# Optimization experiments

Hardware: AMD Instinct MI355X
Metric: run time of the kernel (lower is better)

The kernel has to match this reference:

```python
import jax, jax.numpy as jnp
import numpy as np

N_CLASSES = 91

def setup_inputs() -> dict:
    key = jax.random.key(0)
    k1, k2 = jax.random.split(key)
    B, H, W = 32, 1024, 1024
    inputs = jax.random.randint(k1, (B, H, W), 0, N_CLASSES, dtype=jnp.int32)
    targets = jax.random.randint(k2, (B, H, W), 0, N_CLASSES, dtype=jnp.int32)
    smooth = jnp.ones((1,), dtype=jnp.float32)  # original default smooth=1
    return {"inputs": inputs, "targets": targets, "smooth": smooth}

def reference(inputs, targets, smooth):
    # Single-pass histogram formulation of the original 91-iteration loop.
    B = inputs.shape[0]
    x = inputs.reshape(B, -1)   # [B, N] int labels
    t = targets.reshape(B, -1)  # [B, N]
    rows = jnp.arange(B)[:, None]
    # per-class counts: cnt_x[b,c] = #pixels with x==c (== a.sum per class)
    cnt_x = jnp.zeros((B, N_CLASSES), jnp.float32).at[rows, x].add(1.0)
    cnt_t = jnp.zeros((B, N_CLASSES), jnp.float32).at[rows, t].add(1.0)
    # intersection[b,c] = #pixels with x==t==c; route mismatches to a dump bin
    match = jnp.where(x == t, x, N_CLASSES)
    inter = jnp.zeros((B, N_CLASSES + 1), jnp.float32).at[rows, match].add(1.0)[:, :N_CLASSES]
    union = cnt_x + cnt_t - inter  # total - intersection
    s = smooth[0]
    iou = (inter + s) / (union + s)  # [B, C]
    return iou.mean(axis=1)          # sum_IoU / n_classes, shape [B]
```

## Files before the change

### kernel.cpp

```cpp
#include <hip/hip_runtime.h>

#define NC 91
#define NBIN 182
#define NCOL 8
#define NB 32
#define HW (1024 * 1024)
#define PIX_PER_BLOCK 4096

__global__ __launch_bounds__(256) void hist_kernel(const int* __restrict__ x,
                                                   const int* __restrict__ t,
                                                   int* __restrict__ g_hist) {
    __shared__ int s_h[4][NBIN * NCOL];

    const int tid = threadIdx.x;
    int* sf = &s_h[0][0];
    for (int i = tid; i < 4 * NBIN * NCOL; i += 256) sf[i] = 0;
    __syncthreads();

    const int wave = tid >> 6;
    const int col  = tid & (NCOL - 1);
    int* h = s_h[wave];

    const int b = blockIdx.y;
    const long base = (long)b * HW + (long)blockIdx.x * PIX_PER_BLOCK;
    const int4* __restrict__ x4 = (const int4*)(x + base);
    const int4* __restrict__ t4 = (const int4*)(t + base);

#pragma unroll
    for (int i = 0; i < 4; ++i) {
        int4 xv = x4[i * 256 + tid];
        int4 tv = t4[i * 256 + tid];
        int b0 = xv.x, b1 = xv.y, b2 = xv.z, b3 = xv.w;
        int c0 = (xv.x == tv.x) ? (NC + xv.x) : tv.x;
        int c1 = (xv.y == tv.y) ? (NC + xv.y) : tv.y;
        int c2 = (xv.z == tv.z) ? (NC + xv.z) : tv.z;
        int c3 = (xv.w == tv.w) ? (NC + xv.w) : tv.w;
        atomicAdd(&h[b0 * NCOL + col], 1);
        atomicAdd(&h[c0 * NCOL + col], 1);
        atomicAdd(&h[b1 * NCOL + col], 1);
        atomicAdd(&h[c1 * NCOL + col], 1);
        atomicAdd(&h[b2 * NCOL + col], 1);
        atomicAdd(&h[c2 * NCOL + col], 1);
        atomicAdd(&h[b3 * NCOL + col], 1);
        atomicAdd(&h[c3 * NCOL + col], 1);
    }
    __syncthreads();

    for (int c = tid; c < NBIN; c += 256) {
        int s = 0;
#pragma unroll
        for (int w = 0; w < 4; ++w) {
#pragma unroll
            for (int k = 0; k < NCOL; ++k) s += s_h[w][c * NCOL + k];
        }
        if (s) atomicAdd(&g_hist[b * NBIN + c], s);
    }
}

__global__ __launch_bounds__(64) void finalize_kernel(const int* __restrict__ g_hist,
                                                      const float* __restrict__ smooth,
                                                      float* __restrict__ out) {
    const int b = blockIdx.x;
    const int lane = threadIdx.x;
    const float s = smooth[0];
    float acc = 0.0f;
    for (int c = lane; c < NC; c += 64) {
        float un = (float)g_hist[b * NBIN + c];
        float in = (float)g_hist[b * NBIN + NC + c];
        acc += (in + s) / (un + s);
    }
#pragma unroll
    for (int off = 32; off > 0; off >>= 1)
        acc += __shfl_down(acc, off, 64);
    if (lane == 0) out[b] = acc / (float)NC;
}

extern "C" void kernel_launch(void* const* d_in, const int* in_sizes, int n_in,
                              void* d_out, int out_size, void* d_ws, size_t ws_size,
                              hipStream_t stream) {
    const int* x = (const int*)d_in[0];
    const int* t = (const int*)d_in[1];
    const float* smooth = (const float*)d_in[2];
    float* out = (float*)d_out;

    int* g_hist = (int*)d_ws;

    hipMemsetAsync(d_ws, 0, NB * NBIN * sizeof(int), stream);

    dim3 grid(HW / PIX_PER_BLOCK, NB);
    hist_kernel<<<grid, 256, 0, stream>>>(x, t, g_hist);
    finalize_kernel<<<NB, 64, 0, stream>>>(g_hist, smooth, out);
}
```

Baseline: 281.3 us.

## Use per-thread private byte histograms in LDS instead of shared atomics

Replaces the wave-shared int histograms updated with LDS atomics by a per-thread private histogram of 8-bit counters laid out with a 260-byte stride per bin, so updates are plain non-atomic read-modify-writes. Each block now processes 64 pixels per thread (16384 pixels), which cuts the block count and the number of global atomics. The reduction sums byte counters with udot4 when that builtin is available. Each thread does at most 128 increments per byte, so 8-bit counters cannot overflow. The cost is a larger LDS footprint of about 47KB, which lowers occupancy, plus byte-sized load/store traffic.

```diff
diff --git a/kernel.cpp b/kernel.cpp
--- a/kernel.cpp
+++ b/kernel.cpp
@@ -2,58 +2,66 @@
 
 #define NC 91
 #define NBIN 182
-#define NCOL 8
 #define NB 32
 #define HW (1024 * 1024)
-#define PIX_PER_BLOCK 4096
+#define NT 256
+#define PPT 64
+#define PIX_PER_BLOCK (NT * PPT)
+#define STRIDE 260
 
 __global__ __launch_bounds__(256) void hist_kernel(const int* __restrict__ x,
                                                    const int* __restrict__ t,
                                                    int* __restrict__ g_hist) {
-    __shared__ int s_h[4][NBIN * NCOL];
+    __shared__ unsigned char s_h[NBIN * STRIDE];
 
     const int tid = threadIdx.x;
-    int* sf = &s_h[0][0];
-    for (int i = tid; i < 4 * NBIN * NCOL; i += 256) sf[i] = 0;
+
+    {
+        unsigned int* p = (unsigned int*)s_h;
+        for (int i = tid; i < NBIN * STRIDE / 4; i += NT) p[i] = 0u;
+    }
     __syncthreads();
 
-    const int wave = tid >> 6;
-    const int col  = tid & (NCOL - 1);
-    int* h = s_h[wave];
+    unsigned char* h = s_h + tid;
 
     const int b = blockIdx.y;
     const long base = (long)b * HW + (long)blockIdx.x * PIX_PER_BLOCK;
     const int4* __restrict__ x4 = (const int4*)(x + base);
     const int4* __restrict__ t4 = (const int4*)(t + base);
 
-#pragma unroll
-    for (int i = 0; i < 4; ++i) {
-        int4 xv = x4[i * 256 + tid];
-        int4 tv = t4[i * 256 + tid];
-        int b0 = xv.x, b1 = xv.y, b2 = xv.z, b3 = xv.w;
-        int c0 = (xv.x == tv.x) ? (NC + xv.x) : tv.x;
-        int c1 = (xv.y == tv.y) ? (NC + xv.y) : tv.y;
-        int c2 = (xv.z == tv.z) ? (NC + xv.z) : tv.z;
-        int c3 = (xv.w == tv.w) ? (NC + xv.w) : tv.w;
-        atomicAdd(&h[b0 * NCOL + col], 1);
-        atomicAdd(&h[c0 * NCOL + col], 1);
-        atomicAdd(&h[b1 * NCOL + col], 1);
-        atomicAdd(&h[c1 * NCOL + col], 1);
-        atomicAdd(&h[b2 * NCOL + col], 1);
-        atomicAdd(&h[c2 * NCOL + col], 1);
-        atomicAdd(&h[b3 * NCOL + col], 1);
-        atomicAdd(&h[c3 * NCOL + col], 1);
+#pragma unroll 4
+    for (int i = 0; i < PPT / 4; ++i) {
+        int4 xv = x4[i * NT + tid];
+        int4 tv = t4[i * NT + tid];
+        int u0 = xv.x, u1 = xv.y, u2 = xv.z, u3 = xv.w;
+        int v0 = (xv.x == tv.x) ? (NC + xv.x) : tv.x;
+        int v1 = (xv.y == tv.y) ? (NC + xv.y) : tv.y;
+        int v2 = (xv.z == tv.z) ? (NC + xv.z) : tv.z;
+        int v3 = (xv.w == tv.w) ? (NC + xv.w) : tv.w;
+        h[u0 * STRIDE] += 1;
+        h[v0 * STRIDE] += 1;
+        h[u1 * STRIDE] += 1;
+        h[v1 * STRIDE] += 1;
+        h[u2 * STRIDE] += 1;
+        h[v2 * STRIDE] += 1;
+        h[u3 * STRIDE] += 1;
+        h[v3 * STRIDE] += 1;
     }
     __syncthreads();
 
-    for (int c = tid; c < NBIN; c += 256) {
-        int s = 0;
+    for (int c = tid; c < NBIN; c += NT) {
+        const unsigned int* row = (const unsigned int*)(s_h + c * STRIDE);
+        unsigned int s = 0;
 #pragma unroll
-        for (int w = 0; w < 4; ++w) {
-#pragma unroll
-            for (int k = 0; k < NCOL; ++k) s += s_h[w][c * NCOL + k];
+        for (int k = 0; k < 64; ++k) {
+            unsigned int d = row[k];
+#if __has_builtin(__builtin_amdgcn_udot4)
+            s = __builtin_amdgcn_udot4(d, 0x01010101u, s, false);
+#else
+            s += (d & 0xffu) + ((d >> 8) & 0xffu) + ((d >> 16) & 0xffu) + (d >> 24);
+#endif
         }
-        if (s) atomicAdd(&g_hist[b * NBIN + c], s);
+        atomicAdd(&g_hist[b * NBIN + c], (int)s);
     }
 }
 
@@ -88,6 +96,6 @@
     hipMemsetAsync(d_ws, 0, NB * NBIN * sizeof(int), stream);
 
     dim3 grid(HW / PIX_PER_BLOCK, NB);
-    hist_kernel<<<grid, 256, 0, stream>>>(x, t, g_hist);
+    hist_kernel<<<grid, NT, 0, stream>>>(x, t, g_hist);
     finalize_kernel<<<NB, 64, 0, stream>>>(g_hist, smooth, out);
 }
```

New measurement: 281.2 us. Within noise of the previous version (-0.1%).
